# Kernel optimization log

Measured on AMD Instinct MI355X. Metric: run time of the kernel, lower is better.

## Reference

```python
import jax, jax.numpy as jnp
import numpy as np

N_NODES = 100000
N_EDGES = 1600000
IN_FEATS = 128
NUM_HEADS = 4
OUT_FEATS = 32
NUM_ETYPES = 8
DROP_BLOCKS = 4


def setup_inputs() -> dict:
    key = jax.random.key(0)
    k1, k2, k3, k4, k5 = jax.random.split(key, 5)
    feat = jax.random.normal(k1, (N_NODES, IN_FEATS), dtype=jnp.float32)
    e_feat = jax.random.randint(k2, (N_EDGES,), 0, NUM_ETYPES, dtype=jnp.int32)
    src = jax.random.randint(k3, (N_EDGES,), 0, N_NODES, dtype=jnp.int32)
    dst = jax.random.randint(k4, (N_EDGES,), 0, N_NODES, dtype=jnp.int32)
    kf, ke = jax.random.split(k5)
    # xavier_normal with relu gain for fc: std = gain * sqrt(2/(fan_in+fan_out))
    gain = float(np.sqrt(2.0))
    std = gain * float(np.sqrt(2.0 / (IN_FEATS + NUM_HEADS * OUT_FEATS)))
    fc_weight = jax.random.normal(kf, (NUM_HEADS * OUT_FEATS, IN_FEATS), dtype=jnp.float32) * std
    # edge_emb initialized with normal_()
    edge_emb = jax.random.normal(ke, (NUM_ETYPES, NUM_HEADS), dtype=jnp.float32)
    return {"feat": feat, "fc_weight": fc_weight, "edge_emb": edge_emb,
            "e_feat": e_feat, "src": src, "dst": dst, "drop_blocks": DROP_BLOCKS}


def _edge_softmax(e, dst, n_nodes):
    # segmented softmax over incoming edges per destination node, per head
    # e: (E, H)
    m = jax.ops.segment_max(e, dst, num_segments=n_nodes)      # (N, H)
    z = jnp.exp(e - m[dst])                                    # (E, H)
    s = jax.ops.segment_sum(z, dst, num_segments=n_nodes)      # (N, H)
    return z / s[dst]


def reference(feat, fc_weight, edge_emb, e_feat, src, dst, drop_blocks):
    n = feat.shape[0]
    H = edge_emb.shape[1]
    D = fc_weight.shape[0] // H
    # fc projection -> (N, H, D); feat_drop is identity (p=0 / eval)
    ft = (feat @ fc_weight.T).reshape(n, H, D)
    # edge type embedding logits (E, H)
    ee = edge_emb[e_feat]
    attn = _edge_softmax(ee, dst, n)                           # (E, H)
    # mcdropedge with attn_drop p=0: attn broadcast over blocks is identity scaling
    # u_mul_e + sum: gather src features, scale by attn, scatter-sum into dst
    msg = ft[src] * attn[:, :, None]                           # (E, H, D)
    rst = jax.ops.segment_sum(msg, dst, num_segments=n)        # (N, H, D)
    # attn returned with mcdropedge expansion shape (E, H, drop_blocks, 1)
    attn_out = jnp.broadcast_to(attn[:, :, None], (attn.shape[0], H, drop_blocks))[..., None]
    return rst, attn_out
```

## Files before the change

kernel.cpp:

```cpp
#include <hip/hip_runtime.h>


typedef short short8 __attribute__((ext_vector_type(8)));
typedef float f32x4 __attribute__((ext_vector_type(4)));

__device__ inline unsigned short f2bf(float x) {
    unsigned u = __builtin_bit_cast(unsigned, x);
    u += 0x7FFFu + ((u >> 16) & 1u);
    return (unsigned short)(u >> 16);
}

__global__ __launch_bounds__(256) void k_bcnt(const int* __restrict__ dst,
                                              unsigned* __restrict__ gcnt, int E) {
    __shared__ unsigned l[256];
    int tid = threadIdx.x;
    l[tid] = 0;
    __syncthreads();
    int base = blockIdx.x * 2048;
#pragma unroll
    for (int j = 0; j < 8; ++j) {
        int e = base + j * 256 + tid;
        if (e < E) atomicAdd(&l[(unsigned)dst[e] >> 9], 1u);
    }
    __syncthreads();
    if (l[tid]) atomicAdd(&gcnt[tid], l[tid]);
}

__global__ __launch_bounds__(256) void k_bscan(const unsigned* __restrict__ gcnt,
                                               unsigned* __restrict__ gbase,
                                               unsigned* __restrict__ gcur) {
    __shared__ unsigned s[256];
    int t = threadIdx.x;
    unsigned orig = gcnt[t];
    s[t] = orig;
    __syncthreads();
    for (int of = 1; of < 256; of <<= 1) {
        unsigned v = (t >= of) ? s[t - of] : 0u;
        __syncthreads();
        s[t] += v;
        __syncthreads();
    }
    unsigned eb = s[t] - orig;
    gbase[t] = eb;
    gcur[t] = eb;
}

__global__ __launch_bounds__(256) void k_part(const int* __restrict__ src,
                                              const int* __restrict__ dst,
                                              const int* __restrict__ ef,
                                              unsigned* __restrict__ gcur,
                                              unsigned* __restrict__ csr2,
                                              int E, int nbuk) {
    __shared__ unsigned lcnt[256];
    __shared__ unsigned lbase[256];
    __shared__ unsigned lcur[256];
    __shared__ unsigned gw2[256];
    __shared__ unsigned stp[4096];
    __shared__ unsigned short stb[4096];
    int tid = threadIdx.x;
    lcnt[tid] = 0;
    __syncthreads();

    int cb = blockIdx.x * 4096;
    int cc = E - cb; if (cc > 4096) cc = 4096;

    unsigned pay[16];
    unsigned short bk[16];
#pragma unroll
    for (int j = 0; j < 16; ++j) {
        int idx = j * 256 + tid;
        if (idx < cc) {
            int e = cb + idx;
            unsigned d = (unsigned)dst[e];
            pay[j] = (unsigned)src[e] | ((unsigned)ef[e] << 17) | ((d & 511u) << 20);
            bk[j] = (unsigned short)(d >> 9);
            atomicAdd(&lcnt[bk[j]], 1u);
        }
    }
    __syncthreads();
    lbase[tid] = lcnt[tid];
    __syncthreads();
    for (int of = 1; of < 256; of <<= 1) {
        unsigned v = (tid >= of) ? lbase[tid - of] : 0u;
        __syncthreads();
        lbase[tid] += v;
        __syncthreads();
    }
    unsigned eb = lbase[tid] - lcnt[tid];
    __syncthreads();
    lbase[tid] = eb;
    lcur[tid] = eb;
    __syncthreads();
#pragma unroll
    for (int j = 0; j < 16; ++j) {
        int idx = j * 256 + tid;
        if (idx < cc) {
            unsigned lpos = atomicAdd(&lcur[bk[j]], 1u);
            stp[lpos] = pay[j];
            stb[lpos] = bk[j];
        }
    }
    if (tid < nbuk && lcnt[tid]) gw2[tid] = atomicAdd(&gcur[tid], lcnt[tid]);
    __syncthreads();
#pragma unroll
    for (int j = 0; j < 16; ++j) {
        int i = j * 256 + tid;
        if (i < cc) {
            unsigned b = stb[i];
            csr2[gw2[b] + (i - lbase[b])] = stp[i];
        }
    }
}

__global__ __launch_bounds__(256) void k_bsort2(const unsigned* __restrict__ csr2,
                                                const unsigned* __restrict__ gbase,
                                                const unsigned* __restrict__ gcnt,
                                                const float* __restrict__ emb,
                                                unsigned* __restrict__ csr,
                                                unsigned* __restrict__ offs,
                                                unsigned* __restrict__ deg,
                                                float* __restrict__ stats, int N) {
    __shared__ unsigned cnt8[512 * 8];
    __shared__ unsigned degL[512];
    __shared__ unsigned offsL[512];
    __shared__ unsigned curL[512];
    __shared__ unsigned tmp[256];
    __shared__ float se[32];
    int b = blockIdx.x, tid = threadIdx.x;
    if (tid < 32) se[tid] = emb[tid];
#pragma unroll
    for (int i = 0; i < 16; ++i) cnt8[i * 256 + tid] = 0u;
    __syncthreads();
    unsigned r0 = gbase[b], r1 = r0 + gcnt[b];
    for (unsigned i = r0 + tid; i < r1; i += 256) {
        unsigned en = csr2[i];
        atomicAdd(&cnt8[((en >> 20) & 511u) * 8u + ((en >> 17) & 7u)], 1u);
    }
    __syncthreads();
    int n0 = tid * 2, n1 = tid * 2 + 1;
    unsigned d0 = 0, d1 = 0;
#pragma unroll
    for (int k = 0; k < 8; ++k) { d0 += cnt8[n0 * 8 + k]; d1 += cnt8[n1 * 8 + k]; }
    degL[n0] = d0; degL[n1] = d1;
    tmp[tid] = d0 + d1;
    __syncthreads();
    for (int of = 1; of < 256; of <<= 1) {
        unsigned v = (tid >= of) ? tmp[tid - of] : 0u;
        __syncthreads();
        tmp[tid] += v;
        __syncthreads();
    }
    unsigned eb = tmp[tid] - (d0 + d1);
    offsL[n0] = eb;        curL[n0] = eb;
    offsL[n1] = eb + d0;   curL[n1] = eb + d0;
#pragma unroll
    for (int q = 0; q < 2; ++q) {
        int nl = tid * 2 + q;
        int gn = b * 512 + nl;
        if (gn < N) {
            offs[gn] = r0 + offsL[nl];
            unsigned dg = degL[nl];
            deg[gn] = dg;
            const unsigned* c = &cnt8[nl * 8];
#pragma unroll
            for (int h = 0; h < 4; ++h) {
                float m = -3.4e38f;
#pragma unroll
                for (int tt = 0; tt < 8; ++tt)
                    if (c[tt]) m = fmaxf(m, se[tt * 4 + h]);
                float s = 0.f;
#pragma unroll
                for (int tt = 0; tt < 8; ++tt)
                    if (c[tt]) s += (float)c[tt] * expf(se[tt * 4 + h] - m);
                stats[(size_t)gn * 8 + h] = m;
                stats[(size_t)gn * 8 + 4 + h] = dg ? (1.0f / s) : 0.0f;
            }
        }
    }
    __syncthreads();
    for (unsigned i = r0 + tid; i < r1; i += 256) {
        unsigned en = csr2[i];
        unsigned nlo = (en >> 20) & 511u;
        unsigned tt = (en >> 17) & 7u;
        unsigned pos = r0 + atomicAdd(&curL[nlo], 1u);
        csr[pos] = (en & 0x1FFFFu) | (tt << 20);
    }
}

__global__ void k_attn_out(const int* __restrict__ e_feat, const int* __restrict__ dst,
                           const float* __restrict__ emb, const float* __restrict__ stats,
                           float4* __restrict__ ao, int E4) {
    int i = blockIdx.x * 256 + threadIdx.x;
    if (i >= E4) return;
    int e = i >> 2, h = i & 3;
    int tt = e_feat[e];
    int d = dst[e];
    float a = expf(emb[tt * 4 + h] - stats[(size_t)d * 8 + h]) * stats[(size_t)d * 8 + 4 + h];
    ao[i] = make_float4(a, a, a, a);
}

__global__ __launch_bounds__(256) void k_gemm_mfma(const float* __restrict__ feat,
                                                   const float* __restrict__ W,
                                                   unsigned short* __restrict__ ftb, int N) {
    __shared__ unsigned short As[128 * 128];
    __shared__ unsigned short Bs[128 * 128];
    int tid = threadIdx.x;
    int row0 = blockIdx.x * 128;

#pragma unroll
    for (int it = 0; it < 16; ++it) {
        int i = it * 1024 + tid * 4;
        int r = i >> 7, c = i & 127;
        unsigned swz = (unsigned)((r & 7) << 4);
        float4 w4 = *(const float4*)(W + i);
        ushort4 wb;
        wb.x = f2bf(w4.x); wb.y = f2bf(w4.y); wb.z = f2bf(w4.z); wb.w = f2bf(w4.w);
        *(ushort4*)((char*)Bs + (((unsigned)(r * 256 + c * 2)) ^ swz)) = wb;
        int gr = row0 + r;
        float4 a4 = make_float4(0.f, 0.f, 0.f, 0.f);
        if (gr < N) a4 = *(const float4*)(feat + (size_t)gr * 128 + c);
        ushort4 ab;
        ab.x = f2bf(a4.x); ab.y = f2bf(a4.y); ab.z = f2bf(a4.z); ab.w = f2bf(a4.w);
        *(ushort4*)((char*)As + (((unsigned)(r * 256 + c * 2)) ^ swz)) = ab;
    }
    __syncthreads();

    int wv = tid >> 6, lane = tid & 63;
    int rl = lane & 15;
    unsigned swz = (unsigned)((lane & 7) << 4);
    int kq = (lane >> 4) * 16;

    f32x4 acc[2][8];
#pragma unroll
    for (int rt = 0; rt < 2; ++rt)
#pragma unroll
        for (int jt = 0; jt < 8; ++jt)
            acc[rt][jt] = (f32x4){0.f, 0.f, 0.f, 0.f};

    const char* Ab = (const char*)As;
    const char* Bb = (const char*)Bs;
#pragma unroll
    for (int kk = 0; kk < 4; ++kk) {
        int kb = kk * 64 + kq;
        short8 a[2], bfr[8];
        a[0] = *(const short8*)(Ab + (((unsigned)((wv * 32 + rl) * 256 + kb)) ^ swz));
        a[1] = *(const short8*)(Ab + (((unsigned)((wv * 32 + 16 + rl) * 256 + kb)) ^ swz));
#pragma unroll
        for (int jt = 0; jt < 8; ++jt)
            bfr[jt] = *(const short8*)(Bb + (((unsigned)((jt * 16 + rl) * 256 + kb)) ^ swz));
#pragma unroll
        for (int rt = 0; rt < 2; ++rt)
#pragma unroll
            for (int jt = 0; jt < 8; ++jt)
                acc[rt][jt] = __builtin_amdgcn_mfma_f32_16x16x32_bf16(a[rt], bfr[jt], acc[rt][jt], 0, 0, 0);
    }

#pragma unroll
    for (int rt = 0; rt < 2; ++rt) {
        int gr0 = row0 + wv * 32 + rt * 16 + ((lane >> 4) << 2);
#pragma unroll
        for (int jt = 0; jt < 8; ++jt) {
            int col = jt * 16 + rl;
#pragma unroll
            for (int rg = 0; rg < 4; ++rg) {
                int gr = gr0 + rg;
                if (gr < N) ftb[(size_t)gr * 128 + col] = f2bf(acc[rt][jt][rg]);
            }
        }
    }
}

__global__ __launch_bounds__(256) void k_agg(const unsigned* __restrict__ csr,
                                             const unsigned* __restrict__ offs,
                                             const unsigned* __restrict__ deg,
                                             const float* __restrict__ stats,
                                             const float* __restrict__ emb,
                                             const unsigned* __restrict__ ftu,
                                             float* __restrict__ rst, int N) {
    __shared__ float wl[4 * 32];
    int tid = threadIdx.x;
    int wv = tid >> 6, lane = tid & 63;
    int n = blockIdx.x * 4 + wv;
    n = __builtin_amdgcn_readfirstlane(n);
    if (n < N && lane < 32) {
        int tt = lane >> 2, hh = lane & 3;
        float m = stats[(size_t)n * 8 + hh];
        float is = stats[(size_t)n * 8 + 4 + hh];
        wl[wv * 32 + lane] = expf(emb[tt * 4 + hh] - m) * is;
    }
    __syncthreads();
    if (n >= N) return;
    unsigned o = offs[n], dg = deg[n];
    int h = lane >> 4;
    const float* wlh = wl + wv * 32 + h;
    float accx = 0.f, accy = 0.f;
    unsigned k = o, end = o + dg;
    for (; k + 4 <= end; k += 4) {
        unsigned c0 = csr[k], c1 = csr[k + 1], c2 = csr[k + 2], c3 = csr[k + 3];
        unsigned f0 = ftu[(size_t)(c0 & 0xFFFFFu) * 64 + lane];
        unsigned f1 = ftu[(size_t)(c1 & 0xFFFFFu) * 64 + lane];
        unsigned f2 = ftu[(size_t)(c2 & 0xFFFFFu) * 64 + lane];
        unsigned f3 = ftu[(size_t)(c3 & 0xFFFFFu) * 64 + lane];
        float a0 = wlh[(c0 >> 20) * 4];
        float a1 = wlh[(c1 >> 20) * 4];
        float a2 = wlh[(c2 >> 20) * 4];
        float a3 = wlh[(c3 >> 20) * 4];
        accx = fmaf(a0, __builtin_bit_cast(float, f0 << 16), accx);
        accy = fmaf(a0, __builtin_bit_cast(float, f0 & 0xFFFF0000u), accy);
        accx = fmaf(a1, __builtin_bit_cast(float, f1 << 16), accx);
        accy = fmaf(a1, __builtin_bit_cast(float, f1 & 0xFFFF0000u), accy);
        accx = fmaf(a2, __builtin_bit_cast(float, f2 << 16), accx);
        accy = fmaf(a2, __builtin_bit_cast(float, f2 & 0xFFFF0000u), accy);
        accx = fmaf(a3, __builtin_bit_cast(float, f3 << 16), accx);
        accy = fmaf(a3, __builtin_bit_cast(float, f3 & 0xFFFF0000u), accy);
    }
    for (; k < end; ++k) {
        unsigned c0 = csr[k];
        unsigned f0 = ftu[(size_t)(c0 & 0xFFFFFu) * 64 + lane];
        float a0 = wlh[(c0 >> 20) * 4];
        accx = fmaf(a0, __builtin_bit_cast(float, f0 << 16), accx);
        accy = fmaf(a0, __builtin_bit_cast(float, f0 & 0xFFFF0000u), accy);
    }
    ((float2*)rst)[(size_t)n * 64 + lane] = make_float2(accx, accy);
}

extern "C" void kernel_launch(void* const* d_in, const int* in_sizes, int n_in,
                              void* d_out, int out_size, void* d_ws, size_t ws_size,
                              hipStream_t stream) {
    const float* feat = (const float*)d_in[0];
    const float* W = (const float*)d_in[1];
    const float* emb = (const float*)d_in[2];
    const int* e_feat = (const int*)d_in[3];
    const int* src = (const int*)d_in[4];
    const int* dst = (const int*)d_in[5];
    int N = in_sizes[0] / 128;
    int E = in_sizes[3];
    int nbuk = (N + 511) >> 9;

    char* ws = (char*)d_ws;
    size_t off = 0;
    auto alloc = [&](size_t bytes) {
        void* p = ws + off;
        off = (off + bytes + 255) & ~(size_t)255;
        return p;
    };
    unsigned short* ftb = (unsigned short*)alloc((size_t)N * 128 * 2);
    float* stats = (float*)alloc((size_t)N * 8 * 4);
    unsigned* deg = (unsigned*)alloc((size_t)N * 4);
    unsigned* offs = (unsigned*)alloc((size_t)N * 4);
    unsigned* csr = (unsigned*)alloc((size_t)E * 4);
    unsigned* csr2 = (unsigned*)alloc((size_t)E * 4);
    unsigned* gcnt = (unsigned*)alloc(256 * 4);
    unsigned* gbase = (unsigned*)alloc(256 * 4);
    unsigned* gcur = (unsigned*)alloc(256 * 4);

    float* rst = (float*)d_out;
    float4* ao = (float4*)((float*)d_out + (size_t)N * 128);

    hipMemsetAsync(gcnt, 0, 256 * 4, stream);

    k_bcnt<<<(E + 2047) / 2048, 256, 0, stream>>>(dst, gcnt, E);
    k_bscan<<<1, 256, 0, stream>>>(gcnt, gbase, gcur);
    k_part<<<(E + 4095) / 4096, 256, 0, stream>>>(src, dst, e_feat, gcur, csr2, E, nbuk);
    k_bsort2<<<nbuk, 256, 0, stream>>>(csr2, gbase, gcnt, emb, csr, offs, deg, stats, N);
    k_attn_out<<<(E * 4 + 255) / 256, 256, 0, stream>>>(e_feat, dst, emb, stats, ao, E * 4);
    k_gemm_mfma<<<(N + 127) / 128, 256, 0, stream>>>(feat, W, ftb, N);
    k_agg<<<(N + 3) / 4, 256, 0, stream>>>(csr, offs, deg, stats, emb, (const unsigned*)ftb, rst, N);
}
```

Baseline: 197.4 us.

## Restructure attn_out per-edge, load GEMM A directly, unroll aggregation by eight

k_attn_out now runs one thread per edge instead of one per (edge, head). Each thread reads the destination stats and the embedding row as float4 and writes four float4 outputs, cutting redundant e_feat/dst/stats loads. The GEMM stops staging feat through shared memory: each lane loads its A fragment from global memory and converts it to bf16 in registers, halving LDS use and removing the A-tile writes. The aggregation loop unrolls to eight edges for more memory-level parallelism, and the attn_out launch moves after the GEMM. Per-thread output stores in attn_out become strided across lanes, and the direct global A loads may coalesce less well.

Measured after the change: 198.3 us. About the same (+0.5%).

```diff
diff --git a/kernel.cpp b/kernel.cpp
--- a/kernel.cpp
+++ b/kernel.cpp
@@ -187,22 +187,32 @@
     }
 }
 
-__global__ void k_attn_out(const int* __restrict__ e_feat, const int* __restrict__ dst,
-                           const float* __restrict__ emb, const float* __restrict__ stats,
-                           float4* __restrict__ ao, int E4) {
-    int i = blockIdx.x * 256 + threadIdx.x;
-    if (i >= E4) return;
-    int e = i >> 2, h = i & 3;
+__global__ __launch_bounds__(256) void k_attn_out(const int* __restrict__ e_feat,
+                                                  const int* __restrict__ dst,
+                                                  const float* __restrict__ emb,
+                                                  const float* __restrict__ stats,
+                                                  float4* __restrict__ ao, int E) {
+    int e = blockIdx.x * 256 + threadIdx.x;
+    if (e >= E) return;
     int tt = e_feat[e];
     int d = dst[e];
-    float a = expf(emb[tt * 4 + h] - stats[(size_t)d * 8 + h]) * stats[(size_t)d * 8 + 4 + h];
-    ao[i] = make_float4(a, a, a, a);
+    const float4* st4 = (const float4*)(stats + (size_t)d * 8);
+    float4 m4 = st4[0], i4 = st4[1];
+    float4 ee = *(const float4*)(emb + tt * 4);
+    float a0 = expf(ee.x - m4.x) * i4.x;
+    float a1 = expf(ee.y - m4.y) * i4.y;
+    float a2 = expf(ee.z - m4.z) * i4.z;
+    float a3 = expf(ee.w - m4.w) * i4.w;
+    float4* p = ao + (size_t)e * 4;
+    p[0] = make_float4(a0, a0, a0, a0);
+    p[1] = make_float4(a1, a1, a1, a1);
+    p[2] = make_float4(a2, a2, a2, a2);
+    p[3] = make_float4(a3, a3, a3, a3);
 }
 
 __global__ __launch_bounds__(256) void k_gemm_mfma(const float* __restrict__ feat,
                                                    const float* __restrict__ W,
                                                    unsigned short* __restrict__ ftb, int N) {
-    __shared__ unsigned short As[128 * 128];
     __shared__ unsigned short Bs[128 * 128];
     int tid = threadIdx.x;
     int row0 = blockIdx.x * 128;
@@ -216,12 +226,6 @@
         ushort4 wb;
         wb.x = f2bf(w4.x); wb.y = f2bf(w4.y); wb.z = f2bf(w4.z); wb.w = f2bf(w4.w);
         *(ushort4*)((char*)Bs + (((unsigned)(r * 256 + c * 2)) ^ swz)) = wb;
-        int gr = row0 + r;
-        float4 a4 = make_float4(0.f, 0.f, 0.f, 0.f);
-        if (gr < N) a4 = *(const float4*)(feat + (size_t)gr * 128 + c);
-        ushort4 ab;
-        ab.x = f2bf(a4.x); ab.y = f2bf(a4.y); ab.z = f2bf(a4.z); ab.w = f2bf(a4.w);
-        *(ushort4*)((char*)As + (((unsigned)(r * 256 + c * 2)) ^ swz)) = ab;
     }
     __syncthreads();
 
@@ -229,6 +233,13 @@
     int rl = lane & 15;
     unsigned swz = (unsigned)((lane & 7) << 4);
     int kq = (lane >> 4) * 16;
+    int ko = (lane >> 4) * 8;
+
+    int ra0 = row0 + wv * 32 + rl;
+    int ra1 = ra0 + 16;
+    bool v0 = ra0 < N, v1 = ra1 < N;
+    const float* ap0 = feat + (size_t)ra0 * 128 + ko;
+    const float* ap1 = feat + (size_t)ra1 * 128 + ko;
 
     f32x4 acc[2][8];
 #pragma unroll
@@ -237,14 +248,24 @@
         for (int jt = 0; jt < 8; ++jt)
             acc[rt][jt] = (f32x4){0.f, 0.f, 0.f, 0.f};
 
-    const char* Ab = (const char*)As;
     const char* Bb = (const char*)Bs;
 #pragma unroll
     for (int kk = 0; kk < 4; ++kk) {
         int kb = kk * 64 + kq;
         short8 a[2], bfr[8];
-        a[0] = *(const short8*)(Ab + (((unsigned)((wv * 32 + rl) * 256 + kb)) ^ swz));
-        a[1] = *(const short8*)(Ab + (((unsigned)((wv * 32 + 16 + rl) * 256 + kb)) ^ swz));
+#pragma unroll
+        for (int rt = 0; rt < 2; ++rt) {
+            const float* ap = rt ? ap1 : ap0;
+            bool v = rt ? v1 : v0;
+            float4 lo = make_float4(0.f, 0.f, 0.f, 0.f), hi = lo;
+            if (v) { lo = *(const float4*)(ap + kk * 32); hi = *(const float4*)(ap + kk * 32 + 4); }
+            short8 t;
+            t[0] = (short)f2bf(lo.x); t[1] = (short)f2bf(lo.y);
+            t[2] = (short)f2bf(lo.z); t[3] = (short)f2bf(lo.w);
+            t[4] = (short)f2bf(hi.x); t[5] = (short)f2bf(hi.y);
+            t[6] = (short)f2bf(hi.z); t[7] = (short)f2bf(hi.w);
+            a[rt] = t;
+        }
 #pragma unroll
         for (int jt = 0; jt < 8; ++jt)
             bfr[jt] = *(const short8*)(Bb + (((unsigned)((jt * 16 + rl) * 256 + kb)) ^ swz));
@@ -295,24 +316,18 @@
     const float* wlh = wl + wv * 32 + h;
     float accx = 0.f, accy = 0.f;
     unsigned k = o, end = o + dg;
-    for (; k + 4 <= end; k += 4) {
-        unsigned c0 = csr[k], c1 = csr[k + 1], c2 = csr[k + 2], c3 = csr[k + 3];
-        unsigned f0 = ftu[(size_t)(c0 & 0xFFFFFu) * 64 + lane];
-        unsigned f1 = ftu[(size_t)(c1 & 0xFFFFFu) * 64 + lane];
-        unsigned f2 = ftu[(size_t)(c2 & 0xFFFFFu) * 64 + lane];
-        unsigned f3 = ftu[(size_t)(c3 & 0xFFFFFu) * 64 + lane];
-        float a0 = wlh[(c0 >> 20) * 4];
-        float a1 = wlh[(c1 >> 20) * 4];
-        float a2 = wlh[(c2 >> 20) * 4];
-        float a3 = wlh[(c3 >> 20) * 4];
-        accx = fmaf(a0, __builtin_bit_cast(float, f0 << 16), accx);
-        accy = fmaf(a0, __builtin_bit_cast(float, f0 & 0xFFFF0000u), accy);
-        accx = fmaf(a1, __builtin_bit_cast(float, f1 << 16), accx);
-        accy = fmaf(a1, __builtin_bit_cast(float, f1 & 0xFFFF0000u), accy);
-        accx = fmaf(a2, __builtin_bit_cast(float, f2 << 16), accx);
-        accy = fmaf(a2, __builtin_bit_cast(float, f2 & 0xFFFF0000u), accy);
-        accx = fmaf(a3, __builtin_bit_cast(float, f3 << 16), accx);
-        accy = fmaf(a3, __builtin_bit_cast(float, f3 & 0xFFFF0000u), accy);
+    for (; k + 8 <= end; k += 8) {
+        unsigned c[8], f[8];
+#pragma unroll
+        for (int j = 0; j < 8; ++j) c[j] = csr[k + j];
+#pragma unroll
+        for (int j = 0; j < 8; ++j) f[j] = ftu[(size_t)(c[j] & 0xFFFFFu) * 64 + lane];
+#pragma unroll
+        for (int j = 0; j < 8; ++j) {
+            float a = wlh[(c[j] >> 20) * 4];
+            accx = fmaf(a, __builtin_bit_cast(float, f[j] << 16), accx);
+            accy = fmaf(a, __builtin_bit_cast(float, f[j] & 0xFFFF0000u), accy);
+        }
     }
     for (; k < end; ++k) {
         unsigned c0 = csr[k];
@@ -363,7 +378,7 @@
     k_bscan<<<1, 256, 0, stream>>>(gcnt, gbase, gcur);
     k_part<<<(E + 4095) / 4096, 256, 0, stream>>>(src, dst, e_feat, gcur, csr2, E, nbuk);
     k_bsort2<<<nbuk, 256, 0, stream>>>(csr2, gbase, gcnt, emb, csr, offs, deg, stats, N);
-    k_attn_out<<<(E * 4 + 255) / 256, 256, 0, stream>>>(e_feat, dst, emb, stats, ao, E * 4);
     k_gemm_mfma<<<(N + 127) / 128, 256, 0, stream>>>(feat, W, ftb, N);
+    k_attn_out<<<(E + 255) / 256, 256, 0, stream>>>(e_feat, dst, emb, stats, ao, E);
     k_agg<<<(N + 3) / 4, 256, 0, stream>>>(csr, offs, deg, stats, emb, (const unsigned*)ftb, rst, N);
 }
```
